# Performance work log

Measured on AMD Instinct MI355X. Metric: run time of the kernel, lower is better.

The kernel has to match this reference:

```python
import jax, jax.numpy as jnp
import numpy as np

H = 16        # num_heads
D = 1024      # embed_dim
HD = D // H   # head_dim = 64
B = 8         # batch
L = 128       # tgt_len = rel_len
SCALE = HD ** -0.5


def _rel_shift(r):
    # r: (n, tlen, rlen). Matches torch _rel_shift(zero_tril=True):
    # prepend a column of ONES, reinterpret as (n, rlen+1, tlen), drop first row, tril.
    n, tlen, rlen = r.shape
    zero_pad = jnp.ones((n, tlen, 1), r.dtype)
    r_padded = jnp.concatenate([zero_pad, r], axis=2).reshape(n, rlen + 1, tlen)
    r2 = r_padded[:, 1:, :].reshape(n, tlen, rlen)
    return jnp.tril(r2)


def setup_inputs() -> dict:
    key = jax.random.key(0)
    ks = jax.random.split(key, 9)
    query = jax.random.normal(ks[0], (L, B, D), jnp.float32)
    rel_pe = jax.random.normal(ks[1], (B, L, D), jnp.float32)
    # speaker ids per utterance -> pairwise same-speaker index in {0,1}
    spk = jax.random.randint(ks[2], (B, L), 0, 2)
    causal = jnp.tril(jnp.ones((L, L), jnp.float32))          # valid lower-tri
    umask = causal == 0.0                                       # True = masked
    attn_mask = jnp.broadcast_to(umask[None], (B, L, L))
    attn_mask = jnp.broadcast_to(attn_mask[:, None], (B, H, L, L)).reshape(B * H, L, L)
    spk_mask = ((spk[:, :, None] == spk[:, None, :]) & (~umask)[None]).astype(jnp.int32)
    utt_mask = jnp.broadcast_to(causal[None, :, :, None], (B * H, L, L, 1)).astype(jnp.float32)
    s = 0.03  # ~xavier scale for 1024x1024
    Wq = jax.random.normal(ks[3], (D, D), jnp.float32) * s
    Wk = jax.random.normal(ks[4], (D, D), jnp.float32) * s
    Wv = jax.random.normal(ks[5], (D, D), jnp.float32) * s
    Wr = jax.random.normal(ks[6], (D, D), jnp.float32) * s
    Wo = jax.random.normal(ks[7], (D, D), jnp.float32) * s
    spk_emb = jax.random.normal(ks[8], (2, D), jnp.float32) * 0.05
    return {"query": query, "rel_pe": rel_pe, "utt_mask": utt_mask,
            "Wq": Wq, "Wk": Wk, "Wv": Wv, "Wr": Wr, "Wo": Wo,
            "spk_emb": spk_emb, "attn_mask": attn_mask, "spk_mask": spk_mask}


def reference(query, rel_pe, utt_mask, Wq, Wk, Wv, Wr, Wo, spk_emb, attn_mask, spk_mask):
    Lq, Bq, Dm = query.shape
    # projections (F.linear with bias=None): x @ W^T. NOTE: k/v also from query, as in source.
    q = (query @ Wq.T).reshape(Lq, Bq * H, HD).swapaxes(0, 1)   # (B*H, L, hd)
    k = (query @ Wk.T).reshape(Lq, Bq * H, HD).swapaxes(0, 1)
    v = (query @ Wv.T).reshape(Lq, Bq * H, HD).swapaxes(0, 1)
    r = (rel_pe @ Wr.T).reshape(Lq, Bq * H, HD).swapaxes(0, 1)  # exact torch view semantics
    # s_q: spk_embedding of all-zero ids -> row 0 broadcast, split into heads
    s_q = jnp.broadcast_to(spk_emb[0], (Lq, Bq, Dm)).reshape(Lq, Bq * H, HD).swapaxes(0, 1)
    # s_k: pairwise speaker embedding, exact reshape chain from source
    s_k = spk_emb[spk_mask]                                      # (B, L, L, D)
    s_k = s_k.reshape(Bq, Lq * Lq, Dm).swapaxes(0, 1)            # (L*L, B, D)
    s_k = s_k.reshape(Lq * Lq, Bq * H, HD).swapaxes(0, 1)        # (B*H, L*L, hd)
    s_k = s_k.reshape(Bq * H, Lq, Lq, HD) * utt_mask             # (B*H, L, L, hd)
    new_q = q + s_q
    a1 = jnp.einsum('nid,njd->nij', new_q, k)
    a2 = jnp.einsum('nid,nijd->nij', new_q, s_k)
    a3 = _rel_shift(jnp.einsum('nid,njd->nij', s_q, r))
    scores = (a1 + a2 + a3) * SCALE
    scores = jnp.where(attn_mask, jnp.asarray(1e-30, scores.dtype), scores)
    w = jax.nn.softmax(scores, axis=-1)                          # dropout p=0 (eval)
    out = jnp.einsum('nij,njd->nid', w, v)                       # (B*H, L, hd)
    out = out.swapaxes(0, 1).reshape(Lq, Bq, Dm)
    return out @ Wo.T
```

## Files before the change

### kernel.cpp

```cpp
#include <hip/hip_runtime.h>

#define Dm 1024
#define Lq 128
#define Bq 8
#define Hh 16
#define HDim 64

typedef __attribute__((ext_vector_type(8))) short bf16x8;
typedef __attribute__((ext_vector_type(4))) float f32x4;
typedef unsigned short ushort_t;

__device__ __forceinline__ unsigned short bf16h(float x) {
    unsigned u = __float_as_uint(x);
    return (unsigned short)((u + 0x7FFFu + ((u >> 16) & 1u)) >> 16);
}
__device__ __forceinline__ float bf16f(unsigned short s) {
    return __uint_as_float(((unsigned)s) << 16);
}

__global__ __launch_bounds__(256) void convert5_kernel(
    const float* __restrict__ s0, const float* __restrict__ s1, const float* __restrict__ s2,
    const float* __restrict__ s3, const float* __restrict__ s4,
    ushort_t* __restrict__ d0h, ushort_t* __restrict__ d0l,
    ushort_t* __restrict__ d1h, ushort_t* __restrict__ d1l,
    ushort_t* __restrict__ d2h, ushort_t* __restrict__ d2l,
    ushort_t* __restrict__ d3h, ushort_t* __restrict__ d3l,
    ushort_t* __restrict__ d4h, ushort_t* __restrict__ d4l)
{
    const int z = blockIdx.z;
    const float* src = (z == 0) ? s0 : (z == 1) ? s1 : (z == 2) ? s2 : (z == 3) ? s3 : s4;
    ushort_t* dh = (z == 0) ? d0h : (z == 1) ? d1h : (z == 2) ? d2h : (z == 3) ? d3h : d4h;
    ushort_t* dl = (z == 0) ? d0l : (z == 1) ? d1l : (z == 2) ? d2l : (z == 3) ? d3l : d4l;
    const int idx = (blockIdx.x * 256 + threadIdx.x) * 8;
    const float4 a = *(const float4*)(src + idx);
    const float4 b = *(const float4*)(src + idx + 4);
    float xs[8] = {a.x, a.y, a.z, a.w, b.x, b.y, b.z, b.w};
    unsigned hp[4], lp[4];
    #pragma unroll
    for (int e = 0; e < 4; ++e) {
        unsigned short h0 = bf16h(xs[2*e]), h1 = bf16h(xs[2*e+1]);
        unsigned short l0 = bf16h(xs[2*e]   - bf16f(h0));
        unsigned short l1 = bf16h(xs[2*e+1] - bf16f(h1));
        hp[e] = (unsigned)h0 | ((unsigned)h1 << 16);
        lp[e] = (unsigned)l0 | ((unsigned)l1 << 16);
    }
    *(int4*)(dh + idx) = *(int4*)hp;
    *(int4*)(dl + idx) = *(int4*)lp;
}

__global__ __launch_bounds__(256) void gemm3_kernel(
    const ushort_t* __restrict__ Xhi, const ushort_t* __restrict__ Xlo,
    const ushort_t* __restrict__ W0h, const ushort_t* __restrict__ W0l,
    const ushort_t* __restrict__ W1h, const ushort_t* __restrict__ W1l,
    const ushort_t* __restrict__ W2h, const ushort_t* __restrict__ W2l,
    ushort_t* __restrict__ O0h, ushort_t* __restrict__ O0l,
    ushort_t* __restrict__ O1h, ushort_t* __restrict__ O1l,
    ushort_t* __restrict__ O2h, ushort_t* __restrict__ O2l,
    float* __restrict__ Ofp, const float* __restrict__ bias, int mode)
{
    const int z = blockIdx.z;
    const ushort_t* Wh = (z == 0) ? W0h : (z == 1) ? W1h : W2h;
    const ushort_t* Wl = (z == 0) ? W0l : (z == 1) ? W1l : W2l;
    ushort_t* Ohi = (z == 0) ? O0h : (z == 1) ? O1h : O2h;
    ushort_t* Olo = (z == 0) ? O0l : (z == 1) ? O1l : O2l;

    __shared__ __align__(16) short Axh[2][64][32];
    __shared__ __align__(16) short Axl[2][64][32];
    __shared__ __align__(16) short Bwh[2][64][32];
    __shared__ __align__(16) short Bwl[2][64][32];

    const int t = threadIdx.x, w = t >> 6, l = t & 63;
    const int r0 = blockIdx.y * 64, c0 = blockIdx.x * 64;
    const int wr = w >> 1, wc = w & 1;
    const int srow = t >> 2, sk = (t & 3) * 8;
    const int lr = l & 15, lk = (l >> 4) * 8;

    const size_t xbase = (size_t)(r0 + srow) * Dm + sk;
    const size_t wbase = (size_t)(c0 + srow) * Dm + sk;

    f32x4 acc[2][2];
    #pragma unroll
    for (int m = 0; m < 2; ++m)
        #pragma unroll
        for (int n = 0; n < 2; ++n)
            acc[m][n] = (f32x4){0.f, 0.f, 0.f, 0.f};

    {
        int4 xh = *(const int4*)(Xhi + xbase);
        int4 xl = *(const int4*)(Xlo + xbase);
        int4 wh = *(const int4*)(Wh + wbase);
        int4 wv = *(const int4*)(Wl + wbase);
        *(int4*)&Axh[0][srow][sk] = xh;
        *(int4*)&Axl[0][srow][sk] = xl;
        *(int4*)&Bwh[0][srow][sk] = wh;
        *(int4*)&Bwl[0][srow][sk] = wv;
    }
    __syncthreads();

    int cur = 0;
    for (int step = 0; step < 32; ++step) {
        int4 nxh, nxl, nwh, nwl;
        const bool more = (step < 31);
        if (more) {
            const int kt = (step + 1) * 32;
            nxh = *(const int4*)(Xhi + xbase + kt);
            nxl = *(const int4*)(Xlo + xbase + kt);
            nwh = *(const int4*)(Wh + wbase + kt);
            nwl = *(const int4*)(Wl + wbase + kt);
        }
        bf16x8 ah[2], al[2], bh[2], bl[2];
        #pragma unroll
        for (int m = 0; m < 2; ++m) {
            ah[m] = *(bf16x8*)&Axh[cur][wr * 32 + m * 16 + lr][lk];
            al[m] = *(bf16x8*)&Axl[cur][wr * 32 + m * 16 + lr][lk];
        }
        #pragma unroll
        for (int n = 0; n < 2; ++n) {
            bh[n] = *(bf16x8*)&Bwh[cur][wc * 32 + n * 16 + lr][lk];
            bl[n] = *(bf16x8*)&Bwl[cur][wc * 32 + n * 16 + lr][lk];
        }
        #pragma unroll
        for (int m = 0; m < 2; ++m)
            #pragma unroll
            for (int n = 0; n < 2; ++n) {
                acc[m][n] = __builtin_amdgcn_mfma_f32_16x16x32_bf16(ah[m], bh[n], acc[m][n], 0, 0, 0);
                acc[m][n] = __builtin_amdgcn_mfma_f32_16x16x32_bf16(al[m], bh[n], acc[m][n], 0, 0, 0);
                acc[m][n] = __builtin_amdgcn_mfma_f32_16x16x32_bf16(ah[m], bl[n], acc[m][n], 0, 0, 0);
            }
        if (more) {
            const int nb = cur ^ 1;
            *(int4*)&Axh[nb][srow][sk] = nxh;
            *(int4*)&Axl[nb][srow][sk] = nxl;
            *(int4*)&Bwh[nb][srow][sk] = nwh;
            *(int4*)&Bwl[nb][srow][sk] = nwl;
        }
        __syncthreads();
        cur ^= 1;
    }

    float bz[2] = {0.f, 0.f};
    if (mode == 0 && z == 0 && bias != nullptr) {
        #pragma unroll
        for (int n = 0; n < 2; ++n)
            bz[n] = bias[c0 + wc * 32 + n * 16 + lr];
    }
    #pragma unroll
    for (int m = 0; m < 2; ++m)
        #pragma unroll
        for (int n = 0; n < 2; ++n)
            #pragma unroll
            for (int q = 0; q < 4; ++q) {
                const int r = r0 + wr * 32 + m * 16 + (l >> 4) * 4 + q;
                const int c = c0 + wc * 32 + n * 16 + lr;
                float v = acc[m][n][q] + bz[n];
                const size_t oa = (size_t)r * Dm + c;
                if (mode == 1) {
                    Ofp[oa] = v;
                } else {
                    const unsigned short hh = bf16h(v);
                    Ohi[oa] = hh;
                    Olo[oa] = bf16h(v - bf16f(hh));
                }
            }
}

__global__ __launch_bounds__(256) void wse_kernel(
    const float* __restrict__ Wr, const float* __restrict__ spk_emb,
    float* __restrict__ WSE)
{
    __shared__ float se[64];
    const int t = threadIdx.x;
    const int h = blockIdx.x >> 2;
    const int k = (blockIdx.x & 3) * 256 + t;
    if (t < 64) se[t] = spk_emb[h * 64 + t];
    __syncthreads();
    float s = 0.f;
    #pragma unroll 8
    for (int hd = 0; hd < 64; ++hd)
        s += Wr[(h * 64 + hd) * Dm + k] * se[hd];
    WSE[h * Dm + k] = s;
}

__global__ __launch_bounds__(256) void g_kernel(
    const float* __restrict__ rel_pe, const float* __restrict__ WSE,
    float* __restrict__ G)
{
    __shared__ float rp[1024];
    const int t = threadIdx.x;
    const int p = blockIdx.x;
    ((float4*)rp)[t] = ((const float4*)(rel_pe + p * Dm))[t];
    __syncthreads();
    const int h = t >> 4, part = t & 15;
    float s = 0.f;
    #pragma unroll 8
    for (int m = 0; m < 64; ++m) {
        const int kk = part + (m << 4);
        s += rp[kk] * WSE[h * Dm + kk];
    }
    s += __shfl_down(s, 8, 16);
    s += __shfl_down(s, 4, 16);
    s += __shfl_down(s, 2, 16);
    s += __shfl_down(s, 1, 16);
    if (part == 0) G[p * 16 + h] = s;
}

__global__ __launch_bounds__(256) void transposeV_kernel(
    const ushort_t* __restrict__ Vhi, const ushort_t* __restrict__ Vlo,
    ushort_t* __restrict__ VtHi, ushort_t* __restrict__ VtLo)
{
    __shared__ __align__(16) ushort_t T[128 * 72];
    const int blk = blockIdx.x;
    const int b = blk >> 4, h = blk & 15;
    const ushort_t* src = blockIdx.y ? Vlo : Vhi;
    ushort_t* dst = blockIdx.y ? VtLo : VtHi;
    const int t = threadIdx.x;
    #pragma unroll
    for (int it = 0; it < 4; ++it) {
        const int task = it * 256 + t;
        const int j = task >> 3, hc = (task & 7) * 8;
        *(int4*)&T[j * 72 + hc] = *(const int4*)(src + (size_t)(j * 8 + b) * 1024 + h * 64 + hc);
    }
    __syncthreads();
    #pragma unroll
    for (int it = 0; it < 4; ++it) {
        const int task = it * 256 + t;
        const int hd = task >> 4, jc = (task & 15) * 8;
        ushort_t tmp[8];
        #pragma unroll
        for (int e = 0; e < 8; ++e) tmp[e] = T[(jc + e) * 72 + hd];
        *(int4*)(dst + ((size_t)(b * 16 + h) * 64 + hd) * 128 + jc) = *(int4*)tmp;
    }
}

__global__ __launch_bounds__(256) void attn3_kernel(
    const ushort_t* __restrict__ NQhi, const ushort_t* __restrict__ NQlo,
    const ushort_t* __restrict__ Khi,  const ushort_t* __restrict__ Klo,
    const ushort_t* __restrict__ VtHi, const ushort_t* __restrict__ VtLo,
    const float* __restrict__ G, const int* __restrict__ SM,
    const float* __restrict__ spk_emb,
    ushort_t* __restrict__ Ahi, ushort_t* __restrict__ Alo)
{
    __shared__ __align__(16) ushort_t KP[18432];
    __shared__ __align__(16) ushort_t QV[9216];
    __shared__ float cp[128];
    __shared__ float Es[128];
    __shared__ float se[128];
    __shared__ float zin[64];
    __shared__ unsigned SMw[256];

    const int blk = blockIdx.x, n = blk >> 1, ihalf = blk & 1;
    const int b = n >> 4, h = n & 15;
    const int t = threadIdx.x, w = t >> 6, l = t & 63;
    const int lc = l & 15, lg = l >> 4;
    const int r0w = w * 16;

    ushort_t* Kh = KP;            ushort_t* Kl = KP + 9216;
    ushort_t* Qh = QV;            ushort_t* Ql = QV + 4608;

    #pragma unroll
    for (int it = 0; it < 2; ++it) {
        const int task = it * 256 + t;
        const int r = task >> 3, col = (task & 7) * 8;
        const size_t g0 = (size_t)((ihalf * 64 + r) * 8 + b) * 1024 + h * 64 + col;
        *(int4*)&Qh[r * 72 + col] = *(const int4*)(NQhi + g0);
        *(int4*)&Ql[r * 72 + col] = *(const int4*)(NQlo + g0);
    }
    #pragma unroll
    for (int it = 0; it < 4; ++it) {
        const int task = it * 256 + t;
        const int j = task >> 3, col = (task & 7) * 8;
        const size_t g0 = (size_t)(j * 8 + b) * 1024 + h * 64 + col;
        *(int4*)&Kh[j * 72 + col] = *(const int4*)(Khi + g0);
        *(int4*)&Kl[j * 72 + col] = *(const int4*)(Klo + g0);
    }
    {
        const int r = t >> 2, wd = t & 3;
        const int i_glob = ihalf * 64 + r;
        const int* sp = SM + ((size_t)b * 128 + i_glob) * 128 + wd * 32;
        unsigned bits = 0;
        #pragma unroll
        for (int e8 = 0; e8 < 8; ++e8) {
            const int4 v = *(const int4*)(sp + e8 * 4);
            bits |= (v.x != 0 ? 1u : 0u) << (e8 * 4 + 0);
            bits |= (v.y != 0 ? 1u : 0u) << (e8 * 4 + 1);
            bits |= (v.z != 0 ? 1u : 0u) << (e8 * 4 + 2);
            bits |= (v.w != 0 ? 1u : 0u) << (e8 * 4 + 3);
        }
        SMw[r * 4 + wd] = bits;
    }
    if (t < 128) {
        cp[t] = G[((((t >> 4) << 7) + ((t & 15) << 3) + b) << 4) + h];
        se[t] = spk_emb[(t >> 6) * 1024 + h * 64 + (t & 63)];
    }
    __syncthreads();

    f32x4 acc[8];
    #pragma unroll
    for (int jt = 0; jt < 8; ++jt) acc[jt] = (f32x4){0.f, 0.f, 0.f, 0.f};
    #pragma unroll
    for (int ks = 0; ks < 2; ++ks) {
        const bf16x8 a_h = *(bf16x8*)&Qh[(r0w + lc) * 72 + ks * 32 + lg * 8];
        const bf16x8 a_l = *(bf16x8*)&Ql[(r0w + lc) * 72 + ks * 32 + lg * 8];
        #pragma unroll
        for (int jt = 0; jt < 8; ++jt) {
            const bf16x8 b_h = *(bf16x8*)&Kh[(jt * 16 + lc) * 72 + ks * 32 + lg * 8];
            const bf16x8 b_l = *(bf16x8*)&Kl[(jt * 16 + lc) * 72 + ks * 32 + lg * 8];
            acc[jt] = __builtin_amdgcn_mfma_f32_16x16x32_bf16(a_h, b_h, acc[jt], 0, 0, 0);
            acc[jt] = __builtin_amdgcn_mfma_f32_16x16x32_bf16(a_l, b_h, acc[jt], 0, 0, 0);
            acc[jt] = __builtin_amdgcn_mfma_f32_16x16x32_bf16(a_h, b_l, acc[jt], 0, 0, 0);
        }
    }
    {
        const int r = t >> 2, m = (t >> 1) & 1, half = t & 1;
        float v = 0.f;
        #pragma unroll
        for (int e = 0; e < 32; ++e) {
            const int hd = half * 32 + e;
            const float qf = bf16f(Qh[r * 72 + hd]) + bf16f(Ql[r * 72 + hd]);
            v += qf * se[m * 64 + hd];
        }
        v += __shfl_xor(v, 1);
        if (half == 0) Es[r * 2 + m] = v;
    }
    __syncthreads();

    ushort_t* Ph = KP;            ushort_t* Pl = KP + 8704;
    ushort_t* Vth = QV;           ushort_t* Vtl = QV + 4608;
    #pragma unroll
    for (int q = 0; q < 4; ++q) {
        const int r = r0w + lg * 4 + q;
        const int i_glob = ihalf * 64 + r;
        const float e0 = Es[r * 2 + 0], e1 = Es[r * 2 + 1];
        float s[8];
        #pragma unroll
        for (int jt = 0; jt < 8; ++jt) {
            const int j = jt * 16 + lc;
            if (j > i_glob) {
                s[jt] = 1e-30f;
            } else {
                const unsigned bit = (SMw[r * 4 + (jt >> 1)] >> ((jt & 1) * 16 + lc)) & 1u;
                s[jt] = (acc[jt][q] + (bit ? e1 : e0) + cp[127 + j - i_glob]) * 0.125f;
            }
        }
        float mx = s[0];
        #pragma unroll
        for (int jt = 1; jt < 8; ++jt) mx = fmaxf(mx, s[jt]);
        mx = fmaxf(mx, __shfl_xor(mx, 1));
        mx = fmaxf(mx, __shfl_xor(mx, 2));
        mx = fmaxf(mx, __shfl_xor(mx, 4));
        mx = fmaxf(mx, __shfl_xor(mx, 8));
        float zs = 0.f;
        #pragma unroll
        for (int jt = 0; jt < 8; ++jt) { s[jt] = __expf(s[jt] - mx); zs += s[jt]; }
        zs += __shfl_xor(zs, 1);
        zs += __shfl_xor(zs, 2);
        zs += __shfl_xor(zs, 4);
        zs += __shfl_xor(zs, 8);
        if (lc == 0) zin[r] = 1.f / zs;
        #pragma unroll
        for (int jt = 0; jt < 8; ++jt) {
            const unsigned short hh = bf16h(s[jt]);
            Ph[r * 136 + jt * 16 + lc] = hh;
            Pl[r * 136 + jt * 16 + lc] = bf16h(s[jt] - bf16f(hh));
        }
    }
    #pragma unroll
    for (int it = 0; it < 2; ++it) {
        const int task = it * 256 + t;
        const int hd = task >> 3, jc = (task & 7) * 8;
        const size_t g0 = ((size_t)(b * 16 + h) * 64 + hd) * 128 + jc;
        *(int4*)&Vth[hd * 72 + jc] = *(const int4*)(VtHi + g0);
        *(int4*)&Vtl[hd * 72 + jc] = *(const int4*)(VtLo + g0);
    }
    __syncthreads();

    f32x4 oacc[4];
    #pragma unroll
    for (int nt = 0; nt < 4; ++nt) oacc[nt] = (f32x4){0.f, 0.f, 0.f, 0.f};
    #pragma unroll
    for (int ks = 0; ks < 2; ++ks) {
        const bf16x8 a_h = *(bf16x8*)&Ph[(r0w + lc) * 136 + ks * 32 + lg * 8];
        const bf16x8 a_l = *(bf16x8*)&Pl[(r0w + lc) * 136 + ks * 32 + lg * 8];
        #pragma unroll
        for (int nt = 0; nt < 4; ++nt) {
            const bf16x8 b_h = *(bf16x8*)&Vth[(nt * 16 + lc) * 72 + ks * 32 + lg * 8];
            const bf16x8 b_l = *(bf16x8*)&Vtl[(nt * 16 + lc) * 72 + ks * 32 + lg * 8];
            oacc[nt] = __builtin_amdgcn_mfma_f32_16x16x32_bf16(a_h, b_h, oacc[nt], 0, 0, 0);
            oacc[nt] = __builtin_amdgcn_mfma_f32_16x16x32_bf16(a_l, b_h, oacc[nt], 0, 0, 0);
            oacc[nt] = __builtin_amdgcn_mfma_f32_16x16x32_bf16(a_h, b_l, oacc[nt], 0, 0, 0);
        }
    }
    __syncthreads();

    #pragma unroll
    for (int it = 0; it < 2; ++it) {
        const int task = it * 256 + t;
        const int hd = task >> 3, jc = (task & 7) * 8;
        const size_t g0 = ((size_t)(b * 16 + h) * 64 + hd) * 128 + 64 + jc;
        *(int4*)&Vth[hd * 72 + jc] = *(const int4*)(VtHi + g0);
        *(int4*)&Vtl[hd * 72 + jc] = *(const int4*)(VtLo + g0);
    }
    __syncthreads();

    #pragma unroll
    for (int ks = 0; ks < 2; ++ks) {
        const bf16x8 a_h = *(bf16x8*)&Ph[(r0w + lc) * 136 + 64 + ks * 32 + lg * 8];
        const bf16x8 a_l = *(bf16x8*)&Pl[(r0w + lc) * 136 + 64 + ks * 32 + lg * 8];
        #pragma unroll
        for (int nt = 0; nt < 4; ++nt) {
            const bf16x8 b_h = *(bf16x8*)&Vth[(nt * 16 + lc) * 72 + ks * 32 + lg * 8];
            const bf16x8 b_l = *(bf16x8*)&Vtl[(nt * 16 + lc) * 72 + ks * 32 + lg * 8];
            oacc[nt] = __builtin_amdgcn_mfma_f32_16x16x32_bf16(a_h, b_h, oacc[nt], 0, 0, 0);
            oacc[nt] = __builtin_amdgcn_mfma_f32_16x16x32_bf16(a_l, b_h, oacc[nt], 0, 0, 0);
            oacc[nt] = __builtin_amdgcn_mfma_f32_16x16x32_bf16(a_h, b_l, oacc[nt], 0, 0, 0);
        }
    }
    #pragma unroll
    for (int nt = 0; nt < 4; ++nt)
        #pragma unroll
        for (int q = 0; q < 4; ++q) {
            const int r = r0w + lg * 4 + q;
            const float val = oacc[nt][q] * zin[r];
            const int i_glob = ihalf * 64 + r;
            const size_t oa = (size_t)(i_glob * 8 + b) * 1024 + h * 64 + nt * 16 + lc;
            const unsigned short hh = bf16h(val);
            Ahi[oa] = hh;
            Alo[oa] = bf16h(val - bf16f(hh));
        }
}

extern "C" void kernel_launch(void* const* d_in, const int* in_sizes, int n_in,
                              void* d_out, int out_size, void* d_ws, size_t ws_size,
                              hipStream_t stream) {
    (void)in_sizes; (void)n_in; (void)out_size; (void)ws_size;
    const float* query   = (const float*)d_in[0];
    const float* rel_pe  = (const float*)d_in[1];
    const float* Wq      = (const float*)d_in[3];
    const float* Wk      = (const float*)d_in[4];
    const float* Wv      = (const float*)d_in[5];
    const float* Wr      = (const float*)d_in[6];
    const float* Wo      = (const float*)d_in[7];
    const float* spk_emb = (const float*)d_in[8];
    const int*   SM      = (const int*)d_in[10];
    float* out = (float*)d_out;

    const size_t MB1 = 1u << 20;
    ushort_t* us = (ushort_t*)d_ws;
    ushort_t* qhi  = us + 0 * MB1;   ushort_t* qlo  = us + 1 * MB1;
    ushort_t* wqhi = us + 2 * MB1;   ushort_t* wqlo = us + 3 * MB1;
    ushort_t* wkhi = us + 4 * MB1;   ushort_t* wklo = us + 5 * MB1;
    ushort_t* wvhi = us + 6 * MB1;   ushort_t* wvlo = us + 7 * MB1;
    ushort_t* wohi = us + 8 * MB1;   ushort_t* wolo = us + 9 * MB1;
    ushort_t* nqhi = us + 10 * MB1;  ushort_t* nqlo = us + 11 * MB1;
    ushort_t* khi  = us + 12 * MB1;  ushort_t* klo  = us + 13 * MB1;
    ushort_t* vhi  = us + 14 * MB1;  ushort_t* vlo  = us + 15 * MB1;
    float* WSE = (float*)(us + 16 * MB1);
    float* Gp  = WSE + 16384;
    ushort_t* atthi = qhi;
    ushort_t* attlo = qlo;
    ushort_t* vthi  = wqhi;
    ushort_t* vtlo  = wqlo;

    convert5_kernel<<<dim3(512, 1, 5), 256, 0, stream>>>(
        query, Wq, Wk, Wv, Wo,
        qhi, qlo, wqhi, wqlo, wkhi, wklo, wvhi, wvlo, wohi, wolo);

    gemm3_kernel<<<dim3(16, 16, 3), 256, 0, stream>>>(
        qhi, qlo, wqhi, wqlo, wkhi, wklo, wvhi, wvlo,
        nqhi, nqlo, khi, klo, vhi, vlo, nullptr, spk_emb, 0);

    transposeV_kernel<<<dim3(128, 2), 256, 0, stream>>>(vhi, vlo, vthi, vtlo);
    wse_kernel<<<64, 256, 0, stream>>>(Wr, spk_emb, WSE);
    g_kernel<<<1024, 256, 0, stream>>>(rel_pe, WSE, Gp);

    attn3_kernel<<<256, 256, 0, stream>>>(
        nqhi, nqlo, khi, klo, vthi, vtlo, Gp, SM, spk_emb, atthi, attlo);

    gemm3_kernel<<<dim3(16, 16, 1), 256, 0, stream>>>(
        atthi, attlo, wohi, wolo, wohi, wolo, wohi, wolo,
        nullptr, nullptr, nullptr, nullptr, nullptr, nullptr,
        out, nullptr, 1);
}
```

Measured before the change: 174.3 us.

## Enlarge GEMM tiles to 128x128 and load tiles directly into LDS

After: 200.5 us. +15.0%, slower.

```diff
diff --git a/kernel.cpp b/kernel.cpp
--- a/kernel.cpp
+++ b/kernel.cpp
@@ -9,6 +9,10 @@
 typedef __attribute__((ext_vector_type(8))) short bf16x8;
 typedef __attribute__((ext_vector_type(4))) float f32x4;
 typedef unsigned short ushort_t;
+
+#define GLOAD16(gp, lp) __builtin_amdgcn_global_load_lds( \
+    (const __attribute__((address_space(1))) void*)(gp), \
+    (__attribute__((address_space(3))) void*)(lp), 16, 0, 0)
 
 __device__ __forceinline__ unsigned short bf16h(float x) {
     unsigned u = __float_as_uint(x);
@@ -48,7 +52,7 @@
     *(int4*)(dl + idx) = *(int4*)lp;
 }
 
-__global__ __launch_bounds__(256) void gemm3_kernel(
+__global__ __launch_bounds__(512) void gemm4_kernel(
     const ushort_t* __restrict__ Xhi, const ushort_t* __restrict__ Xlo,
     const ushort_t* __restrict__ W0h, const ushort_t* __restrict__ W0l,
     const ushort_t* __restrict__ W1h, const ushort_t* __restrict__ W1l,
@@ -64,94 +68,75 @@
     ushort_t* Ohi = (z == 0) ? O0h : (z == 1) ? O1h : O2h;
     ushort_t* Olo = (z == 0) ? O0l : (z == 1) ? O1l : O2l;
 
-    __shared__ __align__(16) short Axh[2][64][32];
-    __shared__ __align__(16) short Axl[2][64][32];
-    __shared__ __align__(16) short Bwh[2][64][32];
-    __shared__ __align__(16) short Bwl[2][64][32];
+    __shared__ __align__(16) ushort_t Ah[128 * 32];
+    __shared__ __align__(16) ushort_t Al[128 * 32];
+    __shared__ __align__(16) ushort_t Bh[128 * 32];
+    __shared__ __align__(16) ushort_t Bl[128 * 32];
 
     const int t = threadIdx.x, w = t >> 6, l = t & 63;
-    const int r0 = blockIdx.y * 64, c0 = blockIdx.x * 64;
-    const int wr = w >> 1, wc = w & 1;
-    const int srow = t >> 2, sk = (t & 3) * 8;
-    const int lr = l & 15, lk = (l >> 4) * 8;
-
-    const size_t xbase = (size_t)(r0 + srow) * Dm + sk;
-    const size_t wbase = (size_t)(c0 + srow) * Dm + sk;
-
-    f32x4 acc[2][2];
-    #pragma unroll
-    for (int m = 0; m < 2; ++m)
+    const int r0 = blockIdx.y * 128, c0 = blockIdx.x * 128;
+    const int wr = w >> 2, wc = w & 3;
+    const int lc = l & 15, lg = l >> 4, lk = lg * 8;
+
+    const size_t xg = (size_t)(r0 + (t >> 2)) * Dm + (t & 3) * 8;
+    const size_t wg = (size_t)(c0 + (t >> 2)) * Dm + (t & 3) * 8;
+    ushort_t* la = &Ah[t * 8];
+    ushort_t* lal = &Al[t * 8];
+    ushort_t* lb = &Bh[t * 8];
+    ushort_t* lbl = &Bl[t * 8];
+
+    f32x4 acc[4][2];
+    #pragma unroll
+    for (int m = 0; m < 4; ++m)
         #pragma unroll
         for (int n = 0; n < 2; ++n)
             acc[m][n] = (f32x4){0.f, 0.f, 0.f, 0.f};
 
-    {
-        int4 xh = *(const int4*)(Xhi + xbase);
-        int4 xl = *(const int4*)(Xlo + xbase);
-        int4 wh = *(const int4*)(Wh + wbase);
-        int4 wv = *(const int4*)(Wl + wbase);
-        *(int4*)&Axh[0][srow][sk] = xh;
-        *(int4*)&Axl[0][srow][sk] = xl;
-        *(int4*)&Bwh[0][srow][sk] = wh;
-        *(int4*)&Bwl[0][srow][sk] = wv;
-    }
-    __syncthreads();
-
-    int cur = 0;
-    for (int step = 0; step < 32; ++step) {
-        int4 nxh, nxl, nwh, nwl;
-        const bool more = (step < 31);
-        if (more) {
-            const int kt = (step + 1) * 32;
-            nxh = *(const int4*)(Xhi + xbase + kt);
-            nxl = *(const int4*)(Xlo + xbase + kt);
-            nwh = *(const int4*)(Wh + wbase + kt);
-            nwl = *(const int4*)(Wl + wbase + kt);
-        }
-        bf16x8 ah[2], al[2], bh[2], bl[2];
-        #pragma unroll
-        for (int m = 0; m < 2; ++m) {
-            ah[m] = *(bf16x8*)&Axh[cur][wr * 32 + m * 16 + lr][lk];
-            al[m] = *(bf16x8*)&Axl[cur][wr * 32 + m * 16 + lr][lk];
+    for (int kt = 0; kt < Dm; kt += 32) {
+        __syncthreads();
+        GLOAD16(Xhi + xg + kt, la);
+        GLOAD16(Xlo + xg + kt, lal);
+        GLOAD16(Wh + wg + kt, lb);
+        GLOAD16(Wl + wg + kt, lbl);
+        __syncthreads();
+
+        bf16x8 a_h[4], a_l[4], b_h[2], b_l[2];
+        #pragma unroll
+        for (int m = 0; m < 4; ++m) {
+            const int row = wr * 64 + m * 16 + lc;
+            a_h[m] = *(bf16x8*)&Ah[row * 32 + lk];
+            a_l[m] = *(bf16x8*)&Al[row * 32 + lk];
         }
         #pragma unroll
         for (int n = 0; n < 2; ++n) {
-            bh[n] = *(bf16x8*)&Bwh[cur][wc * 32 + n * 16 + lr][lk];
-            bl[n] = *(bf16x8*)&Bwl[cur][wc * 32 + n * 16 + lr][lk];
-        }
-        #pragma unroll
-        for (int m = 0; m < 2; ++m)
+            const int col = wc * 32 + n * 16 + lc;
+            b_h[n] = *(bf16x8*)&Bh[col * 32 + lk];
+            b_l[n] = *(bf16x8*)&Bl[col * 32 + lk];
+        }
+        #pragma unroll
+        for (int m = 0; m < 4; ++m)
             #pragma unroll
             for (int n = 0; n < 2; ++n) {
-                acc[m][n] = __builtin_amdgcn_mfma_f32_16x16x32_bf16(ah[m], bh[n], acc[m][n], 0, 0, 0);
-                acc[m][n] = __builtin_amdgcn_mfma_f32_16x16x32_bf16(al[m], bh[n], acc[m][n], 0, 0, 0);
-                acc[m][n] = __builtin_amdgcn_mfma_f32_16x16x32_bf16(ah[m], bl[n], acc[m][n], 0, 0, 0);
+                acc[m][n] = __builtin_amdgcn_mfma_f32_16x16x32_bf16(a_h[m], b_h[n], acc[m][n], 0, 0, 0);
+                acc[m][n] = __builtin_amdgcn_mfma_f32_16x16x32_bf16(a_l[m], b_h[n], acc[m][n], 0, 0, 0);
+                acc[m][n] = __builtin_amdgcn_mfma_f32_16x16x32_bf16(a_h[m], b_l[n], acc[m][n], 0, 0, 0);
             }
-        if (more) {
-            const int nb = cur ^ 1;
-            *(int4*)&Axh[nb][srow][sk] = nxh;
-            *(int4*)&Axl[nb][srow][sk] = nxl;
-            *(int4*)&Bwh[nb][srow][sk] = nwh;
-            *(int4*)&Bwl[nb][srow][sk] = nwl;
-        }
-        __syncthreads();
-        cur ^= 1;
     }
 
     float bz[2] = {0.f, 0.f};
     if (mode == 0 && z == 0 && bias != nullptr) {
         #pragma unroll
         for (int n = 0; n < 2; ++n)
-            bz[n] = bias[c0 + wc * 32 + n * 16 + lr];
-    }
-    #pragma unroll
-    for (int m = 0; m < 2; ++m)
+            bz[n] = bias[c0 + wc * 32 + n * 16 + lc];
+    }
+    #pragma unroll
+    for (int m = 0; m < 4; ++m)
         #pragma unroll
         for (int n = 0; n < 2; ++n)
             #pragma unroll
             for (int q = 0; q < 4; ++q) {
-                const int r = r0 + wr * 32 + m * 16 + (l >> 4) * 4 + q;
-                const int c = c0 + wc * 32 + n * 16 + lr;
+                const int r = r0 + wr * 64 + m * 16 + lg * 4 + q;
+                const int c = c0 + wc * 32 + n * 16 + lc;
                 float v = acc[m][n][q] + bz[n];
                 const size_t oa = (size_t)r * Dm + c;
                 if (mode == 1) {
@@ -465,7 +450,7 @@
         query, Wq, Wk, Wv, Wo,
         qhi, qlo, wqhi, wqlo, wkhi, wklo, wvhi, wvlo, wohi, wolo);
 
-    gemm3_kernel<<<dim3(16, 16, 3), 256, 0, stream>>>(
+    gemm4_kernel<<<dim3(8, 8, 3), 512, 0, stream>>>(
         qhi, qlo, wqhi, wqlo, wkhi, wklo, wvhi, wvlo,
         nqhi, nqlo, khi, klo, vhi, vlo, nullptr, spk_emb, 0);
 
@@ -476,7 +461,7 @@
     attn3_kernel<<<256, 256, 0, stream>>>(
         nqhi, nqlo, khi, klo, vthi, vtlo, Gp, SM, spk_emb, atthi, attlo);
 
-    gemm3_kernel<<<dim3(16, 16, 1), 256, 0, stream>>>(
+    gemm4_kernel<<<dim3(8, 8, 1), 512, 0, stream>>>(
         atthi, attlo, wohi, wolo, wohi, wolo, wohi, wolo,
         nullptr, nullptr, nullptr, nullptr, nullptr, nullptr,
         out, nullptr, 1);
```

## Fold V transpose into attention and merge WSE into convert kernel

Applied to the files above, without the earlier changes.

Measured after the change: 168.2 us. -3.5%, faster.

```diff
diff --git a/kernel.cpp b/kernel.cpp
--- a/kernel.cpp
+++ b/kernel.cpp
@@ -18,20 +18,37 @@
     return __uint_as_float(((unsigned)s) << 16);
 }
 
-__global__ __launch_bounds__(256) void convert5_kernel(
+__global__ __launch_bounds__(256) void convert6_kernel(
     const float* __restrict__ s0, const float* __restrict__ s1, const float* __restrict__ s2,
     const float* __restrict__ s3, const float* __restrict__ s4,
     ushort_t* __restrict__ d0h, ushort_t* __restrict__ d0l,
     ushort_t* __restrict__ d1h, ushort_t* __restrict__ d1l,
     ushort_t* __restrict__ d2h, ushort_t* __restrict__ d2l,
     ushort_t* __restrict__ d3h, ushort_t* __restrict__ d3l,
-    ushort_t* __restrict__ d4h, ushort_t* __restrict__ d4l)
+    ushort_t* __restrict__ d4h, ushort_t* __restrict__ d4l,
+    const float* __restrict__ Wr, const float* __restrict__ spk_emb,
+    float* __restrict__ WSE)
 {
     const int z = blockIdx.z;
+    const int t = threadIdx.x;
+    if (z == 5) {
+        if (blockIdx.x >= 64) return;
+        __shared__ float se[64];
+        const int h = blockIdx.x >> 2;
+        const int k = (blockIdx.x & 3) * 256 + t;
+        if (t < 64) se[t] = spk_emb[h * 64 + t];
+        __syncthreads();
+        float s = 0.f;
+        #pragma unroll 8
+        for (int hd = 0; hd < 64; ++hd)
+            s += Wr[(h * 64 + hd) * Dm + k] * se[hd];
+        WSE[h * Dm + k] = s;
+        return;
+    }
     const float* src = (z == 0) ? s0 : (z == 1) ? s1 : (z == 2) ? s2 : (z == 3) ? s3 : s4;
     ushort_t* dh = (z == 0) ? d0h : (z == 1) ? d1h : (z == 2) ? d2h : (z == 3) ? d3h : d4h;
     ushort_t* dl = (z == 0) ? d0l : (z == 1) ? d1l : (z == 2) ? d2l : (z == 3) ? d3l : d4l;
-    const int idx = (blockIdx.x * 256 + threadIdx.x) * 8;
+    const int idx = (blockIdx.x * 256 + t) * 8;
     const float4 a = *(const float4*)(src + idx);
     const float4 b = *(const float4*)(src + idx + 4);
     float xs[8] = {a.x, a.y, a.z, a.w, b.x, b.y, b.z, b.w};
@@ -164,23 +181,6 @@
             }
 }
 
-__global__ __launch_bounds__(256) void wse_kernel(
-    const float* __restrict__ Wr, const float* __restrict__ spk_emb,
-    float* __restrict__ WSE)
-{
-    __shared__ float se[64];
-    const int t = threadIdx.x;
-    const int h = blockIdx.x >> 2;
-    const int k = (blockIdx.x & 3) * 256 + t;
-    if (t < 64) se[t] = spk_emb[h * 64 + t];
-    __syncthreads();
-    float s = 0.f;
-    #pragma unroll 8
-    for (int hd = 0; hd < 64; ++hd)
-        s += Wr[(h * 64 + hd) * Dm + k] * se[hd];
-    WSE[h * Dm + k] = s;
-}
-
 __global__ __launch_bounds__(256) void g_kernel(
     const float* __restrict__ rel_pe, const float* __restrict__ WSE,
     float* __restrict__ G)
@@ -204,38 +204,10 @@
     if (part == 0) G[p * 16 + h] = s;
 }
 
-__global__ __launch_bounds__(256) void transposeV_kernel(
-    const ushort_t* __restrict__ Vhi, const ushort_t* __restrict__ Vlo,
-    ushort_t* __restrict__ VtHi, ushort_t* __restrict__ VtLo)
-{
-    __shared__ __align__(16) ushort_t T[128 * 72];
-    const int blk = blockIdx.x;
-    const int b = blk >> 4, h = blk & 15;
-    const ushort_t* src = blockIdx.y ? Vlo : Vhi;
-    ushort_t* dst = blockIdx.y ? VtLo : VtHi;
-    const int t = threadIdx.x;
-    #pragma unroll
-    for (int it = 0; it < 4; ++it) {
-        const int task = it * 256 + t;
-        const int j = task >> 3, hc = (task & 7) * 8;
-        *(int4*)&T[j * 72 + hc] = *(const int4*)(src + (size_t)(j * 8 + b) * 1024 + h * 64 + hc);
-    }
-    __syncthreads();
-    #pragma unroll
-    for (int it = 0; it < 4; ++it) {
-        const int task = it * 256 + t;
-        const int hd = task >> 4, jc = (task & 15) * 8;
-        ushort_t tmp[8];
-        #pragma unroll
-        for (int e = 0; e < 8; ++e) tmp[e] = T[(jc + e) * 72 + hd];
-        *(int4*)(dst + ((size_t)(b * 16 + h) * 64 + hd) * 128 + jc) = *(int4*)tmp;
-    }
-}
-
-__global__ __launch_bounds__(256) void attn3_kernel(
+__global__ __launch_bounds__(256) void attn4_kernel(
     const ushort_t* __restrict__ NQhi, const ushort_t* __restrict__ NQlo,
     const ushort_t* __restrict__ Khi,  const ushort_t* __restrict__ Klo,
-    const ushort_t* __restrict__ VtHi, const ushort_t* __restrict__ VtLo,
+    const ushort_t* __restrict__ Vhi,  const ushort_t* __restrict__ Vlo,
     const float* __restrict__ G, const int* __restrict__ SM,
     const float* __restrict__ spk_emb,
     ushort_t* __restrict__ Ahi, ushort_t* __restrict__ Alo)
@@ -367,10 +339,17 @@
     #pragma unroll
     for (int it = 0; it < 2; ++it) {
         const int task = it * 256 + t;
-        const int hd = task >> 3, jc = (task & 7) * 8;
-        const size_t g0 = ((size_t)(b * 16 + h) * 64 + hd) * 128 + jc;
-        *(int4*)&Vth[hd * 72 + jc] = *(const int4*)(VtHi + g0);
-        *(int4*)&Vtl[hd * 72 + jc] = *(const int4*)(VtLo + g0);
+        const int j = task >> 3, hc = (task & 7) * 8;
+        const size_t gv = (size_t)(j * 8 + b) * 1024 + h * 64 + hc;
+        int4 uh = *(const int4*)(Vhi + gv);
+        int4 ul = *(const int4*)(Vlo + gv);
+        const ushort_t* ph8 = (const ushort_t*)&uh;
+        const ushort_t* pl8 = (const ushort_t*)&ul;
+        #pragma unroll
+        for (int e = 0; e < 8; ++e) {
+            Vth[(hc + e) * 72 + j] = ph8[e];
+            Vtl[(hc + e) * 72 + j] = pl8[e];
+        }
     }
     __syncthreads();
 
@@ -395,10 +374,17 @@
     #pragma unroll
     for (int it = 0; it < 2; ++it) {
         const int task = it * 256 + t;
-        const int hd = task >> 3, jc = (task & 7) * 8;
-        const size_t g0 = ((size_t)(b * 16 + h) * 64 + hd) * 128 + 64 + jc;
-        *(int4*)&Vth[hd * 72 + jc] = *(const int4*)(VtHi + g0);
-        *(int4*)&Vtl[hd * 72 + jc] = *(const int4*)(VtLo + g0);
+        const int jl = task >> 3, hc = (task & 7) * 8;
+        const size_t gv = (size_t)((64 + jl) * 8 + b) * 1024 + h * 64 + hc;
+        int4 uh = *(const int4*)(Vhi + gv);
+        int4 ul = *(const int4*)(Vlo + gv);
+        const ushort_t* ph8 = (const ushort_t*)&uh;
+        const ushort_t* pl8 = (const ushort_t*)&ul;
+        #pragma unroll
+        for (int e = 0; e < 8; ++e) {
+            Vth[(hc + e) * 72 + jl] = ph8[e];
+            Vtl[(hc + e) * 72 + jl] = pl8[e];
+        }
     }
     __syncthreads();
 
@@ -458,23 +444,20 @@
     float* Gp  = WSE + 16384;
     ushort_t* atthi = qhi;
     ushort_t* attlo = qlo;
-    ushort_t* vthi  = wqhi;
-    ushort_t* vtlo  = wqlo;
-
-    convert5_kernel<<<dim3(512, 1, 5), 256, 0, stream>>>(
+
+    convert6_kernel<<<dim3(512, 1, 6), 256, 0, stream>>>(
         query, Wq, Wk, Wv, Wo,
-        qhi, qlo, wqhi, wqlo, wkhi, wklo, wvhi, wvlo, wohi, wolo);
+        qhi, qlo, wqhi, wqlo, wkhi, wklo, wvhi, wvlo, wohi, wolo,
+        Wr, spk_emb, WSE);
 
     gemm3_kernel<<<dim3(16, 16, 3), 256, 0, stream>>>(
         qhi, qlo, wqhi, wqlo, wkhi, wklo, wvhi, wvlo,
         nqhi, nqlo, khi, klo, vhi, vlo, nullptr, spk_emb, 0);
 
-    transposeV_kernel<<<dim3(128, 2), 256, 0, stream>>>(vhi, vlo, vthi, vtlo);
-    wse_kernel<<<64, 256, 0, stream>>>(Wr, spk_emb, WSE);
     g_kernel<<<1024, 256, 0, stream>>>(rel_pe, WSE, Gp);
 
-    attn3_kernel<<<256, 256, 0, stream>>>(
-        nqhi, nqlo, khi, klo, vthi, vtlo, Gp, SM, spk_emb, atthi, attlo);
+    attn4_kernel<<<256, 256, 0, stream>>>(
+        nqhi, nqlo, khi, klo, vhi, vlo, Gp, SM, spk_emb, atthi, attlo);
 
     gemm3_kernel<<<dim3(16, 16, 1), 256, 0, stream>>>(
         atthi, attlo, wohi, wolo, wohi, wolo, wohi, wolo,
```
